# Kernel tuning notes

Hardware: AMD Instinct MI355X
Metric: run time of the kernel (lower is better)

Reference implementation:

```python
import jax, jax.numpy as jnp
import numpy as np

B, T, D = 2, 1024, 768
H, HS = 12, 64          # n_head, head_size = n_embed // n_head
E, K = 8, 1             # num_experts, top-k (MoeLayer default k=1)
DF = 4 * D              # FFN hidden
EPS = 1e-5


def _ln(x, g, b):
    mu = jnp.mean(x, axis=-1, keepdims=True)
    var = jnp.mean(jnp.square(x - mu), axis=-1, keepdims=True)
    return (x - mu) * jax.lax.rsqrt(var + EPS) * g + b


def setup_inputs() -> dict:
    key = jax.random.key(0)
    ks = jax.random.split(key, 12)
    s = 0.02
    return {
        "x": jax.random.normal(ks[0], (B, T, D), dtype=jnp.float32),
        "ln1_g": jnp.ones((D,), jnp.float32),
        "ln1_b": jnp.zeros((D,), jnp.float32),
        "ln2_g": jnp.ones((D,), jnp.float32),
        "ln2_b": jnp.zeros((D,), jnp.float32),
        "Wq": jax.random.normal(ks[1], (H, D, HS), jnp.float32) * s,
        "Wk": jax.random.normal(ks[2], (H, D, HS), jnp.float32) * s,
        "Wv": jax.random.normal(ks[3], (H, D, HS), jnp.float32) * s,
        "Wp": jax.random.normal(ks[4], (D, D), jnp.float32) * s,
        "bp": jnp.zeros((D,), jnp.float32),
        "Wg": jax.random.normal(ks[5], (D, E), jnp.float32) * s,
        "W1": jax.random.normal(ks[6], (E, D, DF), jnp.float32) * s,
        "b1": jnp.zeros((E, DF), jnp.float32),
        "W2": jax.random.normal(ks[7], (E, DF, D), jnp.float32) * s,
        "b2": jnp.zeros((E, D), jnp.float32),
    }


def reference(x, ln1_g, ln1_b, ln2_g, ln2_b, Wq, Wk, Wv, Wp, bp, Wg, W1, b1, W2, b2):
    b, t, d = x.shape

    # ---- multi-head causal self-attention (per-head QKV, as in Head) ----
    h = _ln(x, ln1_g, ln1_b)
    q = jnp.einsum('btd,hds->bhts', h, Wq)
    k = jnp.einsum('btd,hds->bhts', h, Wk)
    v = jnp.einsum('btd,hds->bhts', h, Wv)
    # NOTE: original scales by C**-0.5 with C = n_embed (not head_size)
    scores = jnp.einsum('bhts,bhus->bhtu', q, k) * (d ** -0.5)
    causal = jnp.tril(jnp.ones((t, t), dtype=bool))
    scores = jnp.where(causal, scores, -jnp.inf)
    att = jax.nn.softmax(scores, axis=-1)
    out = jnp.einsum('bhtu,bhus->bhts', att, v)          # [B,H,T,HS]
    out = out.transpose(0, 2, 1, 3).reshape(b, t, d)     # concat heads
    x = x + out @ Wp + bp

    # ---- top-k MoE feed-forward (MoeLayer, k=1) ----
    h2 = _ln(x, ln2_g, ln2_b).reshape(-1, d)             # [N,D]
    gate_logits = h2 @ Wg                                # [N,E]
    w, sel = jax.lax.top_k(gate_logits, K)               # [N,K]
    w = jax.nn.softmax(w.astype(jnp.float32), axis=-1).astype(x.dtype)
    n = h2.shape[0]
    combine = jnp.zeros((n, Wg.shape[1]), x.dtype).at[
        jnp.arange(n)[:, None], sel].add(w)              # [N,E]
    hid = jax.nn.relu(jnp.einsum('nd,edf->enf', h2, W1) + b1[:, None, :])
    y = jnp.einsum('enf,efd->end', hid, W2) + b2[:, None, :]
    moe = jnp.einsum('ne,end->nd', combine, y)           # dense dispatch
    return x + moe.reshape(b, t, d)
```

## Files before the change

### kernel.cpp

```cpp
#include <hip/hip_runtime.h>
#include <math.h>

typedef __bf16 bf16;
typedef __bf16 bf16x4 __attribute__((ext_vector_type(4)));
typedef __bf16 bf16x8 __attribute__((ext_vector_type(8)));
typedef float f32x4 __attribute__((ext_vector_type(4)));

#define N_TOK 2048
#define DMODEL 768
#define NHEAD 12
#define TSEQ 1024
#define NEXP 8
#define DFF 3072

__device__ inline f32x4 mfma16(bf16x8 a, bf16x8 b, f32x4 c) {
    return __builtin_amdgcn_mfma_f32_16x16x32_bf16(a, b, c, 0, 0, 0);
}

__device__ inline f32x4 zero4() { f32x4 z = {0.f, 0.f, 0.f, 0.f}; return z; }

__device__ inline float block_sum(float v, float* red, int tid) {
#pragma unroll
    for (int off = 32; off > 0; off >>= 1) v += __shfl_down(v, off, 64);
    __syncthreads();
    if ((tid & 63) == 0) red[tid >> 6] = v;
    __syncthreads();
    return red[0] + red[1] + red[2] + red[3];
}

__global__ __launch_bounds__(256) void ln1_kernel(const float* __restrict__ x,
        const float* __restrict__ g, const float* __restrict__ b,
        bf16* __restrict__ hh, bf16* __restrict__ hl,
        int* __restrict__ cz, float* __restrict__ outz) {
    __shared__ float red[4];
    int row = blockIdx.x, tid = threadIdx.x;
    if (row == 0 && tid < 16) cz[tid] = 0;
#pragma unroll
    for (int i = 0; i < 3; i++) outz[(size_t)row * DMODEL + tid + i * 256] = 0.f;
    const float* xr = x + (size_t)row * DMODEL;
    float v[3];
#pragma unroll
    for (int i = 0; i < 3; i++) v[i] = xr[tid + i * 256];
    float s = block_sum(v[0] + v[1] + v[2], red, tid);
    float mu = s * (1.f / DMODEL);
    float q = 0.f;
#pragma unroll
    for (int i = 0; i < 3; i++) { float d = v[i] - mu; q += d * d; }
    q = block_sum(q, red, tid);
    float rstd = 1.0f / sqrtf(q * (1.f / DMODEL) + 1e-5f);
#pragma unroll
    for (int i = 0; i < 3; i++) {
        int d = tid + i * 256;
        float val = (v[i] - mu) * rstd * g[d] + b[d];
        bf16 hi = (bf16)val;
        hh[(size_t)row * DMODEL + d] = hi;
        hl[(size_t)row * DMODEL + d] = (bf16)(val - (float)hi);
    }
}

__device__ inline void gemm_step3(const bf16* lah, const bf16* lal,
                                  const bf16* lbh, const bf16* lbl,
                                  int wm, int wn, int row16, int quad,
                                  f32x4 acc[4][4]) {
    bf16x8 ah[4], al[4], bh[4], bl[4];
#pragma unroll
    for (int i = 0; i < 4; i++) {
        int ro = (wm * 64 + i * 16 + row16) * 40 + quad * 8;
        ah[i] = *(const bf16x8*)&lah[ro];
        al[i] = *(const bf16x8*)&lal[ro];
    }
#pragma unroll
    for (int i = 0; i < 4; i++) {
        int ro = (wn * 64 + i * 16 + row16) * 40 + quad * 8;
        bh[i] = *(const bf16x8*)&lbh[ro];
        bl[i] = *(const bf16x8*)&lbl[ro];
    }
#pragma unroll
    for (int mi = 0; mi < 4; mi++)
#pragma unroll
        for (int ni = 0; ni < 4; ni++) {
            acc[mi][ni] = mfma16(ah[mi], bh[ni], acc[mi][ni]);
            acc[mi][ni] = mfma16(ah[mi], bl[ni], acc[mi][ni]);
            acc[mi][ni] = mfma16(al[mi], bh[ni], acc[mi][ni]);
        }
}

__device__ inline void gemm_step1(const bf16* la, const bf16* lb, int wm, int wn,
                                  int row16, int quad, f32x4 acc[4][4]) {
    bf16x8 af[4], bfr[4];
#pragma unroll
    for (int i = 0; i < 4; i++)
        af[i] = *(const bf16x8*)&la[(wm * 64 + i * 16 + row16) * 40 + quad * 8];
#pragma unroll
    for (int i = 0; i < 4; i++)
        bfr[i] = *(const bf16x8*)&lb[(wn * 64 + i * 16 + row16) * 40 + quad * 8];
#pragma unroll
    for (int mi = 0; mi < 4; mi++)
#pragma unroll
        for (int ni = 0; ni < 4; ni++)
            acc[mi][ni] = mfma16(af[mi], bfr[ni], acc[mi][ni]);
}

#define TILE_E (128 * 40)

__device__ inline void wstore_hilo(bf16* lbh, bf16* lbl, int base, const float* wv) {
#pragma unroll
    for (int gq = 0; gq < 4; gq++) {
        bf16x4 ph, pl;
#pragma unroll
        for (int j = 0; j < 4; j++) {
            float v = wv[gq * 4 + j];
            bf16 hi = (bf16)v;
            ph[j] = hi;
            pl[j] = (bf16)(v - (float)hi);
        }
        *(bf16x4*)&lbh[base + gq * 4] = ph;
        *(bf16x4*)&lbl[base + gq * 4] = pl;
    }
}
__device__ inline void wstore1(bf16* lb, int base, const float* wv) {
#pragma unroll
    for (int gq = 0; gq < 4; gq++) {
        bf16x4 p;
#pragma unroll
        for (int j = 0; j < 4; j++) p[j] = (bf16)wv[gq * 4 + j];
        *(bf16x4*)&lb[base + gq * 4] = p;
    }
}

__global__ __launch_bounds__(256) void qkv_gemm(const bf16* __restrict__ hA_h,
        const bf16* __restrict__ hA_l,
        const float* __restrict__ Wq, const float* __restrict__ Wk,
        const float* __restrict__ Wv,
        bf16* __restrict__ qh, bf16* __restrict__ ql,
        bf16* __restrict__ kh, bf16* __restrict__ kl,
        bf16* __restrict__ vh, bf16* __restrict__ vl) {
    __shared__ alignas(16) bf16 lah[2 * TILE_E];
    __shared__ alignas(16) bf16 lal[2 * TILE_E];
    __shared__ alignas(16) bf16 lbh[2 * TILE_E];
    __shared__ alignas(16) bf16 lbl[2 * TILE_E];
    int id = blockIdx.x;
    int nt = id % 24;
    if (nt >= 18) return;
    int m0 = (id / 24) * 128;
    int tid = threadIdx.x;
    int sel = nt / 6;
    int n0 = (nt % 6) * 128;
    const float* W = (sel == 0) ? Wq : (sel == 1) ? Wk : Wv;
    bf16* obh = (sel == 0) ? qh : (sel == 1) ? kh : vh;
    bf16* obl = (sel == 0) ? ql : (sel == 1) ? kl : vl;
    int lane = tid & 63, w = tid >> 6, row16 = lane & 15, quad = lane >> 4;
    int wm = w >> 1, wn = w & 1;
    int r_a = tid >> 2, c_a = (tid & 3) << 3;
    int nW = tid & 127, kb16 = (tid >> 7) * 16;
    size_t wcol = (size_t)((n0 + nW) >> 6) * DMODEL * 64 + ((n0 + nW) & 63);
    int wbase = nW * 40 + kb16;
    f32x4 acc[4][4];
#pragma unroll
    for (int mi = 0; mi < 4; mi++)
#pragma unroll
        for (int ni = 0; ni < 4; ni++) acc[mi][ni] = zero4();
    const bf16* Ah = hA_h + (size_t)m0 * DMODEL;
    const bf16* Al = hA_l + (size_t)m0 * DMODEL;
    bf16x8 rAh0_0, rAh1_0, rAl0_0, rAl1_0, rAh0_1, rAh1_1, rAl0_1, rAl1_1;
    float wv0[16], wv1[16];

#define QK_LOAD(bk, k0) do { \
    rAh0_##bk = *(const bf16x8*)&Ah[(size_t)r_a * DMODEL + (k0) + c_a]; \
    rAh1_##bk = *(const bf16x8*)&Ah[(size_t)(r_a + 64) * DMODEL + (k0) + c_a]; \
    rAl0_##bk = *(const bf16x8*)&Al[(size_t)r_a * DMODEL + (k0) + c_a]; \
    rAl1_##bk = *(const bf16x8*)&Al[(size_t)(r_a + 64) * DMODEL + (k0) + c_a]; \
    _Pragma("unroll") for (int i = 0; i < 16; i++) \
        wv##bk[i] = W[wcol + (size_t)((k0) + kb16 + i) * 64]; \
} while (0)
#define QK_STORE(bk, lofs) do { \
    *(bf16x8*)&lah[(lofs) + r_a * 40 + c_a] = rAh0_##bk; \
    *(bf16x8*)&lah[(lofs) + (r_a + 64) * 40 + c_a] = rAh1_##bk; \
    *(bf16x8*)&lal[(lofs) + r_a * 40 + c_a] = rAl0_##bk; \
    *(bf16x8*)&lal[(lofs) + (r_a + 64) * 40 + c_a] = rAl1_##bk; \
    wstore_hilo(lbh + (lofs), lbl + (lofs), wbase, wv##bk); \
} while (0)

    const int nk = DMODEL / 32;
    QK_LOAD(0, 0);
    QK_LOAD(1, 32);
    QK_STORE(0, 0);
    for (int ki = 0; ki < nk; ki += 2) {
        __syncthreads();
        if (ki + 2 < nk) QK_LOAD(0, (ki + 2) * 32);
        gemm_step3(lah, lal, lbh, lbl, wm, wn, row16, quad, acc);
        QK_STORE(1, TILE_E);
        __syncthreads();
        if (ki + 3 < nk) QK_LOAD(1, (ki + 3) * 32);
        gemm_step3(lah + TILE_E, lal + TILE_E, lbh + TILE_E, lbl + TILE_E,
                   wm, wn, row16, quad, acc);
        if (ki + 2 < nk) QK_STORE(0, 0);
    }
#undef QK_LOAD
#undef QK_STORE
#pragma unroll
    for (int mi = 0; mi < 4; mi++) {
        int rowl = wm * 64 + mi * 16 + quad * 4;
#pragma unroll
        for (int ni = 0; ni < 4; ni++) {
            int col = n0 + wn * 64 + ni * 16 + row16;
            int hhd = col >> 6, s = col & 63;
#pragma unroll
            for (int r = 0; r < 4; r++) {
                int gm = m0 + rowl + r;
                int bb = gm >> 10, t = gm & 1023;
                size_t oi = (((size_t)bb * NHEAD + hhd) * TSEQ + t) * 64 + s;
                float val = acc[mi][ni][r];
                bf16 hi = (bf16)val;
                obh[oi] = hi;
                obl[oi] = (bf16)(val - (float)hi);
            }
        }
    }
}

__global__ __launch_bounds__(256) void attn_kernel(const bf16* __restrict__ qhb,
        const bf16* __restrict__ qlb, const bf16* __restrict__ khb,
        const bf16* __restrict__ klb, const bf16* __restrict__ vhb,
        const bf16* __restrict__ vlb, bf16* __restrict__ aoh,
        bf16* __restrict__ aol) {
    __shared__ alignas(16) bf16 kt_h[64 * 72];
    __shared__ alignas(16) bf16 kt_l[64 * 72];
    __shared__ alignas(16) bf16 vt_h[64 * 72];
    __shared__ alignas(16) bf16 vt_l[64 * 72];
    __shared__ alignas(16) bf16 p_h[4][16 * 72];
    __shared__ alignas(16) bf16 p_l[4][16 * 72];
    int qt = blockIdx.x, bh = blockIdx.y;
    int b = bh / NHEAD, hh = bh % NHEAD;
    int tid = threadIdx.x, lane = tid & 63, w = tid >> 6;
    int row16 = lane & 15, quad = lane >> 4;
    const bf16* qph = qhb + (size_t)bh * TSEQ * 64;
    const bf16* qpl = qlb + (size_t)bh * TSEQ * 64;
    const bf16* kph = khb + (size_t)bh * TSEQ * 64;
    const bf16* kpl = klb + (size_t)bh * TSEQ * 64;
    const bf16* vph = vhb + (size_t)bh * TSEQ * 64;
    const bf16* vpl = vlb + (size_t)bh * TSEQ * 64;
    int qrow = qt * 64 + w * 16 + row16;
    bf16x8 aq_h[2], aq_l[2];
#pragma unroll
    for (int kk = 0; kk < 2; kk++) {
        aq_h[kk] = *(const bf16x8*)&qph[(size_t)qrow * 64 + kk * 32 + quad * 8];
        aq_l[kk] = *(const bf16x8*)&qpl[(size_t)qrow * 64 + kk * 32 + quad * 8];
    }
    f32x4 o[4];
    float m_i[4], l_i[4];
#pragma unroll
    for (int i = 0; i < 4; i++) { o[i] = zero4(); m_i[i] = -INFINITY; l_i[i] = 0.f; }
    const float sc = 0.03608439182435161f;
    for (int kt = 0; kt <= qt; kt++) {
        __syncthreads();
#pragma unroll
        for (int i = 0; i < 2; i++) {
            int chunk = tid + i * 256;
            int r = chunk >> 3, c = (chunk & 7) << 3;
            size_t gi = (size_t)(kt * 64 + r) * 64 + c;
            *(bf16x8*)&kt_h[r * 72 + c] = *(const bf16x8*)&kph[gi];
            *(bf16x8*)&kt_l[r * 72 + c] = *(const bf16x8*)&kpl[gi];
        }
#pragma unroll
        for (int u = 0; u < 4; u++) {
            int unit = tid + u * 256;
            int s = unit & 63, tg = unit >> 6;
            bf16x4 ph, pl;
#pragma unroll
            for (int j = 0; j < 4; j++) {
                size_t gi = (size_t)(kt * 64 + tg * 4 + j) * 64 + s;
                ph[j] = vph[gi];
                pl[j] = vpl[gi];
            }
            *(bf16x4*)&vt_h[s * 72 + tg * 4] = ph;
            *(bf16x4*)&vt_l[s * 72 + tg * 4] = pl;
        }
        __syncthreads();
        f32x4 sacc[4];
#pragma unroll
        for (int ni = 0; ni < 4; ni++) {
            sacc[ni] = zero4();
#pragma unroll
            for (int kk = 0; kk < 2; kk++) {
                int ro = (ni * 16 + row16) * 72 + kk * 32 + quad * 8;
                bf16x8 bk_h = *(const bf16x8*)&kt_h[ro];
                bf16x8 bk_l = *(const bf16x8*)&kt_l[ro];
                sacc[ni] = mfma16(aq_h[kk], bk_h, sacc[ni]);
                sacc[ni] = mfma16(aq_h[kk], bk_l, sacc[ni]);
                sacc[ni] = mfma16(aq_l[kk], bk_h, sacc[ni]);
            }
        }
        float mrow[4];
#pragma unroll
        for (int r = 0; r < 4; r++) mrow[r] = -INFINITY;
        int tq_b = qt * 64 + w * 16 + quad * 4;
#pragma unroll
        for (int ni = 0; ni < 4; ni++) {
            int tkg = kt * 64 + ni * 16 + row16;
#pragma unroll
            for (int r = 0; r < 4; r++) {
                float sv = sacc[ni][r] * sc;
                if (tkg > tq_b + r) sv = -INFINITY;
                sacc[ni][r] = sv;
                mrow[r] = fmaxf(mrow[r], sv);
            }
        }
#pragma unroll
        for (int r = 0; r < 4; r++) {
#pragma unroll
            for (int off = 8; off > 0; off >>= 1)
                mrow[r] = fmaxf(mrow[r], __shfl_xor(mrow[r], off, 16));
        }
        float alpha[4], rsum[4];
#pragma unroll
        for (int r = 0; r < 4; r++) {
            float nm = fmaxf(m_i[r], mrow[r]);
            alpha[r] = __expf(m_i[r] - nm);
            m_i[r] = nm;
            rsum[r] = 0.f;
        }
#pragma unroll
        for (int ni = 0; ni < 4; ni++)
#pragma unroll
            for (int r = 0; r < 4; r++) {
                float p = __expf(sacc[ni][r] - m_i[r]);
                sacc[ni][r] = p;
                rsum[r] += p;
            }
#pragma unroll
        for (int r = 0; r < 4; r++) {
#pragma unroll
            for (int off = 8; off > 0; off >>= 1)
                rsum[r] += __shfl_xor(rsum[r], off, 16);
            l_i[r] = l_i[r] * alpha[r] + rsum[r];
        }
#pragma unroll
        for (int ni = 0; ni < 4; ni++)
#pragma unroll
            for (int r = 0; r < 4; r++) o[ni][r] *= alpha[r];
#pragma unroll
        for (int ni = 0; ni < 4; ni++)
#pragma unroll
            for (int r = 0; r < 4; r++) {
                float p = sacc[ni][r];
                bf16 hi = (bf16)p;
                int po = (quad * 4 + r) * 72 + ni * 16 + row16;
                p_h[w][po] = hi;
                p_l[w][po] = (bf16)(p - (float)hi);
            }
        __syncthreads();
        bf16x8 ap_h[2], ap_l[2];
#pragma unroll
        for (int kk = 0; kk < 2; kk++) {
            ap_h[kk] = *(const bf16x8*)&p_h[w][row16 * 72 + kk * 32 + quad * 8];
            ap_l[kk] = *(const bf16x8*)&p_l[w][row16 * 72 + kk * 32 + quad * 8];
        }
#pragma unroll
        for (int ni = 0; ni < 4; ni++)
#pragma unroll
            for (int kk = 0; kk < 2; kk++) {
                int ro = (ni * 16 + row16) * 72 + kk * 32 + quad * 8;
                bf16x8 bv_h = *(const bf16x8*)&vt_h[ro];
                bf16x8 bv_l = *(const bf16x8*)&vt_l[ro];
                o[ni] = mfma16(ap_h[kk], bv_h, o[ni]);
                o[ni] = mfma16(ap_h[kk], bv_l, o[ni]);
                o[ni] = mfma16(ap_l[kk], bv_h, o[ni]);
            }
    }
    int t = qt * 64 + w * 16 + quad * 4;
#pragma unroll
    for (int ni = 0; ni < 4; ni++) {
        int col = hh * 64 + ni * 16 + row16;
#pragma unroll
        for (int r = 0; r < 4; r++) {
            float val = o[ni][r] / l_i[r];
            size_t n = (size_t)b * TSEQ + t + r;
            bf16 hi = (bf16)val;
            aoh[n * DMODEL + col] = hi;
            aol[n * DMODEL + col] = (bf16)(val - (float)hi);
        }
    }
}

__global__ __launch_bounds__(256) void proj_gemm(const bf16* __restrict__ aInH,
        const bf16* __restrict__ aInL,
        const float* __restrict__ Wp, const float* __restrict__ bp,
        const float* __restrict__ x, float* __restrict__ x1) {
    __shared__ alignas(16) bf16 lah[2 * TILE_E];
    __shared__ alignas(16) bf16 lal[2 * TILE_E];
    __shared__ alignas(16) bf16 lbh[2 * TILE_E];
    __shared__ alignas(16) bf16 lbl[2 * TILE_E];
    int id = blockIdx.x;
    int n0t = id & 7;
    if (n0t >= 6) return;
    int m0 = (id >> 3) * 128, n0 = n0t * 128;
    int tid = threadIdx.x;
    int lane = tid & 63, w = tid >> 6, row16 = lane & 15, quad = lane >> 4;
    int wm = w >> 1, wn = w & 1;
    int r_a = tid >> 2, c_a = (tid & 3) << 3;
    int nW = tid & 127, kb16 = (tid >> 7) * 16;
    int wbase = nW * 40 + kb16;
    f32x4 acc[4][4];
#pragma unroll
    for (int mi = 0; mi < 4; mi++)
#pragma unroll
        for (int ni = 0; ni < 4; ni++) acc[mi][ni] = zero4();
    const bf16* Ah = aInH + (size_t)m0 * DMODEL;
    const bf16* Al = aInL + (size_t)m0 * DMODEL;
    bf16x8 rAh0_0, rAh1_0, rAl0_0, rAl1_0, rAh0_1, rAh1_1, rAl0_1, rAl1_1;
    float wv0[16], wv1[16];

#define PJ_LOAD(bk, k0) do { \
    rAh0_##bk = *(const bf16x8*)&Ah[(size_t)r_a * DMODEL + (k0) + c_a]; \
    rAh1_##bk = *(const bf16x8*)&Ah[(size_t)(r_a + 64) * DMODEL + (k0) + c_a]; \
    rAl0_##bk = *(const bf16x8*)&Al[(size_t)r_a * DMODEL + (k0) + c_a]; \
    rAl1_##bk = *(const bf16x8*)&Al[(size_t)(r_a + 64) * DMODEL + (k0) + c_a]; \
    _Pragma("unroll") for (int i = 0; i < 16; i++) \
        wv##bk[i] = Wp[(size_t)((k0) + kb16 + i) * DMODEL + n0 + nW]; \
} while (0)
#define PJ_STORE(bk, lofs) do { \
    *(bf16x8*)&lah[(lofs) + r_a * 40 + c_a] = rAh0_##bk; \
    *(bf16x8*)&lah[(lofs) + (r_a + 64) * 40 + c_a] = rAh1_##bk; \
    *(bf16x8*)&lal[(lofs) + r_a * 40 + c_a] = rAl0_##bk; \
    *(bf16x8*)&lal[(lofs) + (r_a + 64) * 40 + c_a] = rAl1_##bk; \
    wstore_hilo(lbh + (lofs), lbl + (lofs), wbase, wv##bk); \
} while (0)

    const int nk = DMODEL / 32;
    PJ_LOAD(0, 0);
    PJ_LOAD(1, 32);
    PJ_STORE(0, 0);
    for (int ki = 0; ki < nk; ki += 2) {
        __syncthreads();
        if (ki + 2 < nk) PJ_LOAD(0, (ki + 2) * 32);
        gemm_step3(lah, lal, lbh, lbl, wm, wn, row16, quad, acc);
        PJ_STORE(1, TILE_E);
        __syncthreads();
        if (ki + 3 < nk) PJ_LOAD(1, (ki + 3) * 32);
        gemm_step3(lah + TILE_E, lal + TILE_E, lbh + TILE_E, lbl + TILE_E,
                   wm, wn, row16, quad, acc);
        if (ki + 2 < nk) PJ_STORE(0, 0);
    }
#undef PJ_LOAD
#undef PJ_STORE
#pragma unroll
    for (int mi = 0; mi < 4; mi++) {
        int rowl = wm * 64 + mi * 16 + quad * 4;
#pragma unroll
        for (int ni = 0; ni < 4; ni++) {
            int col = n0 + wn * 64 + ni * 16 + row16;
#pragma unroll
            for (int r = 0; r < 4; r++) {
                int gm = m0 + rowl + r;
                x1[(size_t)gm * DMODEL + col] =
                    acc[mi][ni][r] + bp[col] + x[(size_t)gm * DMODEL + col];
            }
        }
    }
}

__global__ __launch_bounds__(256) void ln2_gate_kernel(const float* __restrict__ x1,
        const float* __restrict__ g, const float* __restrict__ b,
        const float* __restrict__ Wg, bf16* __restrict__ h2,
        int* __restrict__ sel, int* __restrict__ counts) {
    __shared__ float red[4];
    __shared__ float glog[8];
    int row = blockIdx.x, tid = threadIdx.x;
    if (tid < 8) glog[tid] = 0.f;
    const float* xr = x1 + (size_t)row * DMODEL;
    float v[3];
#pragma unroll
    for (int i = 0; i < 3; i++) v[i] = xr[tid + i * 256];
    float s = block_sum(v[0] + v[1] + v[2], red, tid);
    float mu = s * (1.f / DMODEL);
    float qv = 0.f;
#pragma unroll
    for (int i = 0; i < 3; i++) { float d = v[i] - mu; qv += d * d; }
    qv = block_sum(qv, red, tid);
    float rstd = 1.0f / sqrtf(qv * (1.f / DMODEL) + 1e-5f);
    float ga[8];
#pragma unroll
    for (int e = 0; e < 8; e++) ga[e] = 0.f;
#pragma unroll
    for (int i = 0; i < 3; i++) {
        int d = tid + i * 256;
        float hv = (v[i] - mu) * rstd * g[d] + b[d];
        h2[(size_t)row * DMODEL + d] = (bf16)hv;
        const float* wgr = Wg + (size_t)d * NEXP;
#pragma unroll
        for (int e = 0; e < 8; e++) ga[e] += hv * wgr[e];
    }
#pragma unroll
    for (int e = 0; e < 8; e++)
#pragma unroll
        for (int off = 32; off > 0; off >>= 1) ga[e] += __shfl_down(ga[e], off, 64);
    if ((tid & 63) == 0)
#pragma unroll
        for (int e = 0; e < 8; e++) atomicAdd(&glog[e], ga[e]);
    __syncthreads();
    if (tid == 0) {
        float best = glog[0];
        int bi = 0;
#pragma unroll
        for (int e = 1; e < 8; e++)
            if (glog[e] > best) { best = glog[e]; bi = e; }
        sel[row] = bi;
        atomicAdd(&counts[bi], 1);
    }
}

__global__ void scatter_kernel(const int* __restrict__ sel, const int* __restrict__ counts,
                               int* __restrict__ cursor, int* __restrict__ perm) {
    int n = blockIdx.x * blockDim.x + threadIdx.x;
    if (n >= N_TOK) return;
    int e = sel[n];
    int off = 0;
    for (int i = 0; i < NEXP; i++) off += (i < e) ? counts[i] : 0;
    int pos = atomicAdd(&cursor[e], 1);
    perm[off + pos] = n;
}

__global__ __launch_bounds__(256) void moe1_gemm(const bf16* __restrict__ h2,
        const float* __restrict__ W1, const float* __restrict__ b1,
        const int* __restrict__ counts, const int* __restrict__ perm,
        bf16* __restrict__ hid) {
    int e = blockIdx.z;
    int cnt = counts[e];
    int rt = blockIdx.y;
    if (rt * 128 >= cnt) return;
    int off = 0;
    for (int i = 0; i < NEXP; i++) off += (i < e) ? counts[i] : 0;
    int n0 = blockIdx.x * 128;
    const float* W = W1 + (size_t)e * DMODEL * DFF;
    __shared__ alignas(16) bf16 la[2 * TILE_E];
    __shared__ alignas(16) bf16 lb[2 * TILE_E];
    int tid = threadIdx.x;
    int lane = tid & 63, w = tid >> 6, row16 = lane & 15, quad = lane >> 4;
    int wm = w >> 1, wn = w & 1;
    int r_a = tid >> 2, c_a = (tid & 3) << 3;
    int nW = tid & 127, kb16 = (tid >> 7) * 16;
    int wbase = nW * 40 + kb16;
    int tok0 = perm[off + min(rt * 128 + r_a, cnt - 1)];
    int tok1 = perm[off + min(rt * 128 + r_a + 64, cnt - 1)];
    const bf16* a0 = h2 + (size_t)tok0 * DMODEL;
    const bf16* a1 = h2 + (size_t)tok1 * DMODEL;
    f32x4 acc[4][4];
#pragma unroll
    for (int mi = 0; mi < 4; mi++)
#pragma unroll
        for (int ni = 0; ni < 4; ni++) acc[mi][ni] = zero4();
    bf16x8 rA0_0, rA1_0, rA0_1, rA1_1;
    float wv0[16], wv1[16];

#define M1_LOAD(bk, k0) do { \
    rA0_##bk = *(const bf16x8*)&a0[(k0) + c_a]; \
    rA1_##bk = *(const bf16x8*)&a1[(k0) + c_a]; \
    _Pragma("unroll") for (int i = 0; i < 16; i++) \
        wv##bk[i] = W[(size_t)((k0) + kb16 + i) * DFF + n0 + nW]; \
} while (0)
#define M1_STORE(bk, lofs) do { \
    *(bf16x8*)&la[(lofs) + r_a * 40 + c_a] = rA0_##bk; \
    *(bf16x8*)&la[(lofs) + (r_a + 64) * 40 + c_a] = rA1_##bk; \
    wstore1(lb + (lofs), wbase, wv##bk); \
} while (0)

    const int nk = DMODEL / 32;
    M1_LOAD(0, 0);
    M1_LOAD(1, 32);
    M1_STORE(0, 0);
    for (int ki = 0; ki < nk; ki += 2) {
        __syncthreads();
        if (ki + 2 < nk) M1_LOAD(0, (ki + 2) * 32);
        gemm_step1(la, lb, wm, wn, row16, quad, acc);
        M1_STORE(1, TILE_E);
        __syncthreads();
        if (ki + 3 < nk) M1_LOAD(1, (ki + 3) * 32);
        gemm_step1(la + TILE_E, lb + TILE_E, wm, wn, row16, quad, acc);
        if (ki + 2 < nk) M1_STORE(0, 0);
    }
#undef M1_LOAD
#undef M1_STORE
#pragma unroll
    for (int mi = 0; mi < 4; mi++) {
        int rowl = wm * 64 + mi * 16 + quad * 4;
#pragma unroll
        for (int ni = 0; ni < 4; ni++) {
            int col = n0 + wn * 64 + ni * 16 + row16;
#pragma unroll
            for (int r = 0; r < 4; r++) {
                int lr = rowl + r;
                if (rt * 128 + lr < cnt) {
                    float val = acc[mi][ni][r] + b1[(size_t)e * DFF + col];
                    val = fmaxf(val, 0.f);
                    hid[(size_t)(off + rt * 128 + lr) * DFF + col] = (bf16)val;
                }
            }
        }
    }
}

__global__ __launch_bounds__(256) void moe2_gemm(const bf16* __restrict__ hid,
        const float* __restrict__ W2, const float* __restrict__ b2,
        const int* __restrict__ counts, const int* __restrict__ perm,
        const float* __restrict__ x1, float* __restrict__ out) {
    int id = blockIdx.x;
    int n0t = id & 7;
    if (n0t >= 6) return;
    int rt = (id >> 3) & 15;
    int ez = id >> 7;
    int e = ez & 7, ks = ez >> 3;
    int cnt = counts[e];
    if (rt * 128 >= cnt) return;
    int off = 0;
    for (int i = 0; i < NEXP; i++) off += (i < e) ? counts[i] : 0;
    int n0 = n0t * 128;
    const float* W = W2 + (size_t)e * DFF * DMODEL;
    __shared__ alignas(16) bf16 la[2 * TILE_E];
    __shared__ alignas(16) bf16 lb[2 * TILE_E];
    int tid = threadIdx.x;
    int lane = tid & 63, w = tid >> 6, row16 = lane & 15, quad = lane >> 4;
    int wm = w >> 1, wn = w & 1;
    int r_a = tid >> 2, c_a = (tid & 3) << 3;
    int nW = tid & 127, kb16 = (tid >> 7) * 16;
    int wbase = nW * 40 + kb16;
    const int kst = ks * (DFF / 4);
    const bf16* a0 = hid + (size_t)min(off + rt * 128 + r_a, N_TOK - 1) * DFF + kst;
    const bf16* a1 = hid + (size_t)min(off + rt * 128 + r_a + 64, N_TOK - 1) * DFF + kst;
    const float* Wk_ = W + (size_t)kst * DMODEL;
    f32x4 acc[4][4];
#pragma unroll
    for (int mi = 0; mi < 4; mi++)
#pragma unroll
        for (int ni = 0; ni < 4; ni++) acc[mi][ni] = zero4();
    bf16x8 rA0_0, rA1_0, rA0_1, rA1_1;
    float wv0[16], wv1[16];

#define M2_LOAD(bk, k0) do { \
    rA0_##bk = *(const bf16x8*)&a0[(k0) + c_a]; \
    rA1_##bk = *(const bf16x8*)&a1[(k0) + c_a]; \
    _Pragma("unroll") for (int i = 0; i < 16; i++) \
        wv##bk[i] = Wk_[(size_t)((k0) + kb16 + i) * DMODEL + n0 + nW]; \
} while (0)
#define M2_STORE(bk, lofs) do { \
    *(bf16x8*)&la[(lofs) + r_a * 40 + c_a] = rA0_##bk; \
    *(bf16x8*)&la[(lofs) + (r_a + 64) * 40 + c_a] = rA1_##bk; \
    wstore1(lb + (lofs), wbase, wv##bk); \
} while (0)

    const int nk = (DFF / 4) / 32;
    M2_LOAD(0, 0);
    M2_LOAD(1, 32);
    M2_STORE(0, 0);
    for (int ki = 0; ki < nk; ki += 2) {
        __syncthreads();
        if (ki + 2 < nk) M2_LOAD(0, (ki + 2) * 32);
        gemm_step1(la, lb, wm, wn, row16, quad, acc);
        M2_STORE(1, TILE_E);
        __syncthreads();
        if (ki + 3 < nk) M2_LOAD(1, (ki + 3) * 32);
        gemm_step1(la + TILE_E, lb + TILE_E, wm, wn, row16, quad, acc);
        if (ki + 2 < nk) M2_STORE(0, 0);
    }
#undef M2_LOAD
#undef M2_STORE
#pragma unroll
    for (int mi = 0; mi < 4; mi++) {
        int rowl = wm * 64 + mi * 16 + quad * 4;
#pragma unroll
        for (int ni = 0; ni < 4; ni++) {
            int col = n0 + wn * 64 + ni * 16 + row16;
#pragma unroll
            for (int r = 0; r < 4; r++) {
                int lr = rowl + r;
                if (rt * 128 + lr < cnt) {
                    int n = perm[off + rt * 128 + lr];
                    float val = acc[mi][ni][r];
                    if (ks == 0)
                        val += b2[(size_t)e * DMODEL + col] + x1[(size_t)n * DMODEL + col];
                    atomicAdd(&out[(size_t)n * DMODEL + col], val);
                }
            }
        }
    }
}

extern "C" void kernel_launch(void* const* d_in, const int* in_sizes, int n_in,
                              void* d_out, int out_size, void* d_ws, size_t ws_size,
                              hipStream_t stream) {
    const float* x    = (const float*)d_in[0];
    const float* ln1g = (const float*)d_in[1];
    const float* ln1b = (const float*)d_in[2];
    const float* ln2g = (const float*)d_in[3];
    const float* ln2b = (const float*)d_in[4];
    const float* Wq   = (const float*)d_in[5];
    const float* Wk   = (const float*)d_in[6];
    const float* Wv   = (const float*)d_in[7];
    const float* Wp   = (const float*)d_in[8];
    const float* bp   = (const float*)d_in[9];
    const float* Wg   = (const float*)d_in[10];
    const float* W1   = (const float*)d_in[11];
    const float* b1   = (const float*)d_in[12];
    const float* W2   = (const float*)d_in[13];
    const float* b2   = (const float*)d_in[14];
    float* out = (float*)d_out;

    char* ws = (char*)d_ws;
    size_t off = 0;
    const size_t SZ = (size_t)N_TOK * DMODEL * 2;
    bf16* h1h = (bf16*)(ws + off); off += SZ;
    bf16* h1l = (bf16*)(ws + off); off += SZ;
    bf16* qh  = (bf16*)(ws + off); off += SZ;
    bf16* ql  = (bf16*)(ws + off); off += SZ;
    bf16* kh  = (bf16*)(ws + off); off += SZ;
    bf16* kl  = (bf16*)(ws + off); off += SZ;
    bf16* vh  = (bf16*)(ws + off); off += SZ;
    bf16* vl  = (bf16*)(ws + off); off += SZ;
    bf16* aoh = (bf16*)(ws + off); off += SZ;
    bf16* aol = (bf16*)(ws + off); off += SZ;
    float* x1 = (float*)(ws + off); off += (size_t)N_TOK * DMODEL * 4;
    bf16* h2  = (bf16*)(ws + off); off += SZ;
    bf16* hid = (bf16*)(ws + off); off += (size_t)N_TOK * DFF * 2;
    int* counts  = (int*)(ws + off); off += 8 * 4;
    int* cursor  = (int*)(ws + off); off += 8 * 4;
    int* sel     = (int*)(ws + off); off += (size_t)N_TOK * 4;
    int* perm    = (int*)(ws + off); off += (size_t)N_TOK * 4;

    ln1_kernel<<<N_TOK, 256, 0, stream>>>(x, ln1g, ln1b, h1h, h1l, counts, out);
    qkv_gemm<<<24 * 16, 256, 0, stream>>>(h1h, h1l, Wq, Wk, Wv, qh, ql, kh, kl, vh, vl);
    attn_kernel<<<dim3(16, 24), 256, 0, stream>>>(qh, ql, kh, kl, vh, vl, aoh, aol);
    proj_gemm<<<8 * 16, 256, 0, stream>>>(aoh, aol, Wp, bp, x, x1);
    ln2_gate_kernel<<<N_TOK, 256, 0, stream>>>(x1, ln2g, ln2b, Wg, h2, sel, counts);
    scatter_kernel<<<8, 256, 0, stream>>>(sel, counts, cursor, perm);
    moe1_gemm<<<dim3(24, 16, 8), 256, 0, stream>>>(h2, W1, b1, counts, perm, hid);
    moe2_gemm<<<8 * 16 * 32, 256, 0, stream>>>(hid, W2, b2, counts, perm, x1, out);
}
```

Baseline: 625.5 us.

## Pre-pack MoE expert weights into bf16 tiled layout and simplify GEMM pipelines

Adds a pack_w kernel that runs every call and converts the fp32 W1/W2 expert weights into bf16, transposed and tiled into contiguous 32x128 blocks. The MoE GEMMs then load B tiles with two vectorized 16-byte loads per thread instead of sixteen strided fp32 loads, and they no longer convert to bf16 inside the loop. All GEMM main loops are also restructured from a two-register-set, two-step unrolled pipeline to a single register set with ping-pong shared-memory buffers, which lowers register pressure. The cost is that packing reads and writes all expert weights each call, roughly 150MB fp32 read, even though only the routed experts' rows are used.

```diff
diff --git a/kernel.cpp b/kernel.cpp
--- a/kernel.cpp
+++ b/kernel.cpp
@@ -58,6 +58,37 @@
     }
 }
 
+__global__ __launch_bounds__(256) void pack_w(const float* __restrict__ src,
+        bf16* __restrict__ dst, int K, int N) {
+    int kt = blockIdx.x, nt = blockIdx.y, e = blockIdx.z;
+    int nkt = gridDim.x;
+    const float* S = src + ((size_t)e * K + kt * 32) * N + nt * 128;
+    bf16* D = dst + (((size_t)e * gridDim.y + nt) * nkt + kt) * 4096;
+    __shared__ float t[32][129];
+    int tid = threadIdx.x;
+    int kk = tid >> 4, nn = (tid & 15) * 8;
+#pragma unroll
+    for (int h = 0; h < 2; h++) {
+        int k = kk + 16 * h;
+        float4 v0 = *(const float4*)&S[(size_t)k * N + nn];
+        float4 v1 = *(const float4*)&S[(size_t)k * N + nn + 4];
+        t[k][nn + 0] = v0.x; t[k][nn + 1] = v0.y;
+        t[k][nn + 2] = v0.z; t[k][nn + 3] = v0.w;
+        t[k][nn + 4] = v1.x; t[k][nn + 5] = v1.y;
+        t[k][nn + 6] = v1.z; t[k][nn + 7] = v1.w;
+    }
+    __syncthreads();
+    int n = tid >> 1, kh = (tid & 1) * 16;
+    bf16x8 o0, o1;
+#pragma unroll
+    for (int j = 0; j < 8; j++) {
+        o0[j] = (bf16)t[kh + j][n];
+        o1[j] = (bf16)t[kh + 8 + j][n];
+    }
+    *(bf16x8*)&D[n * 32 + kh] = o0;
+    *(bf16x8*)&D[n * 32 + kh + 8] = o1;
+}
+
 __device__ inline void gemm_step3(const bf16* lah, const bf16* lal,
                                   const bf16* lbh, const bf16* lbl,
                                   int wm, int wn, int row16, int quad,
@@ -116,15 +147,6 @@
         }
         *(bf16x4*)&lbh[base + gq * 4] = ph;
         *(bf16x4*)&lbl[base + gq * 4] = pl;
-    }
-}
-__device__ inline void wstore1(bf16* lb, int base, const float* wv) {
-#pragma unroll
-    for (int gq = 0; gq < 4; gq++) {
-        bf16x4 p;
-#pragma unroll
-        for (int j = 0; j < 4; j++) p[j] = (bf16)wv[gq * 4 + j];
-        *(bf16x4*)&lb[base + gq * 4] = p;
     }
 }
 
@@ -162,39 +184,34 @@
         for (int ni = 0; ni < 4; ni++) acc[mi][ni] = zero4();
     const bf16* Ah = hA_h + (size_t)m0 * DMODEL;
     const bf16* Al = hA_l + (size_t)m0 * DMODEL;
-    bf16x8 rAh0_0, rAh1_0, rAl0_0, rAl1_0, rAh0_1, rAh1_1, rAl0_1, rAl1_1;
-    float wv0[16], wv1[16];
-
-#define QK_LOAD(bk, k0) do { \
-    rAh0_##bk = *(const bf16x8*)&Ah[(size_t)r_a * DMODEL + (k0) + c_a]; \
-    rAh1_##bk = *(const bf16x8*)&Ah[(size_t)(r_a + 64) * DMODEL + (k0) + c_a]; \
-    rAl0_##bk = *(const bf16x8*)&Al[(size_t)r_a * DMODEL + (k0) + c_a]; \
-    rAl1_##bk = *(const bf16x8*)&Al[(size_t)(r_a + 64) * DMODEL + (k0) + c_a]; \
+    bf16x8 rAh0, rAh1, rAl0, rAl1;
+    float wv[16];
+
+#define QK_LOAD(k0) do { \
+    rAh0 = *(const bf16x8*)&Ah[(size_t)r_a * DMODEL + (k0) + c_a]; \
+    rAh1 = *(const bf16x8*)&Ah[(size_t)(r_a + 64) * DMODEL + (k0) + c_a]; \
+    rAl0 = *(const bf16x8*)&Al[(size_t)r_a * DMODEL + (k0) + c_a]; \
+    rAl1 = *(const bf16x8*)&Al[(size_t)(r_a + 64) * DMODEL + (k0) + c_a]; \
     _Pragma("unroll") for (int i = 0; i < 16; i++) \
-        wv##bk[i] = W[wcol + (size_t)((k0) + kb16 + i) * 64]; \
+        wv[i] = W[wcol + (size_t)((k0) + kb16 + i) * 64]; \
 } while (0)
-#define QK_STORE(bk, lofs) do { \
-    *(bf16x8*)&lah[(lofs) + r_a * 40 + c_a] = rAh0_##bk; \
-    *(bf16x8*)&lah[(lofs) + (r_a + 64) * 40 + c_a] = rAh1_##bk; \
-    *(bf16x8*)&lal[(lofs) + r_a * 40 + c_a] = rAl0_##bk; \
-    *(bf16x8*)&lal[(lofs) + (r_a + 64) * 40 + c_a] = rAl1_##bk; \
-    wstore_hilo(lbh + (lofs), lbl + (lofs), wbase, wv##bk); \
+#define QK_STORE(lofs) do { \
+    *(bf16x8*)&lah[(lofs) + r_a * 40 + c_a] = rAh0; \
+    *(bf16x8*)&lah[(lofs) + (r_a + 64) * 40 + c_a] = rAh1; \
+    *(bf16x8*)&lal[(lofs) + r_a * 40 + c_a] = rAl0; \
+    *(bf16x8*)&lal[(lofs) + (r_a + 64) * 40 + c_a] = rAl1; \
+    wstore_hilo(lbh + (lofs), lbl + (lofs), wbase, wv); \
 } while (0)
 
     const int nk = DMODEL / 32;
-    QK_LOAD(0, 0);
-    QK_LOAD(1, 32);
-    QK_STORE(0, 0);
-    for (int ki = 0; ki < nk; ki += 2) {
+    QK_LOAD(0);
+    QK_STORE(0);
+    for (int ki = 0; ki < nk; ki++) {
         __syncthreads();
-        if (ki + 2 < nk) QK_LOAD(0, (ki + 2) * 32);
-        gemm_step3(lah, lal, lbh, lbl, wm, wn, row16, quad, acc);
-        QK_STORE(1, TILE_E);
-        __syncthreads();
-        if (ki + 3 < nk) QK_LOAD(1, (ki + 3) * 32);
-        gemm_step3(lah + TILE_E, lal + TILE_E, lbh + TILE_E, lbl + TILE_E,
-                   wm, wn, row16, quad, acc);
-        if (ki + 2 < nk) QK_STORE(0, 0);
+        int cur = (ki & 1) * TILE_E, nxt = ((ki + 1) & 1) * TILE_E;
+        if (ki + 1 < nk) QK_LOAD((ki + 1) * 32);
+        gemm_step3(lah + cur, lal + cur, lbh + cur, lbl + cur, wm, wn, row16, quad, acc);
+        if (ki + 1 < nk) QK_STORE(nxt);
     }
 #undef QK_LOAD
 #undef QK_STORE
@@ -408,39 +425,34 @@
         for (int ni = 0; ni < 4; ni++) acc[mi][ni] = zero4();
     const bf16* Ah = aInH + (size_t)m0 * DMODEL;
     const bf16* Al = aInL + (size_t)m0 * DMODEL;
-    bf16x8 rAh0_0, rAh1_0, rAl0_0, rAl1_0, rAh0_1, rAh1_1, rAl0_1, rAl1_1;
-    float wv0[16], wv1[16];
-
-#define PJ_LOAD(bk, k0) do { \
-    rAh0_##bk = *(const bf16x8*)&Ah[(size_t)r_a * DMODEL + (k0) + c_a]; \
-    rAh1_##bk = *(const bf16x8*)&Ah[(size_t)(r_a + 64) * DMODEL + (k0) + c_a]; \
-    rAl0_##bk = *(const bf16x8*)&Al[(size_t)r_a * DMODEL + (k0) + c_a]; \
-    rAl1_##bk = *(const bf16x8*)&Al[(size_t)(r_a + 64) * DMODEL + (k0) + c_a]; \
+    bf16x8 rAh0, rAh1, rAl0, rAl1;
+    float wv[16];
+
+#define PJ_LOAD(k0) do { \
+    rAh0 = *(const bf16x8*)&Ah[(size_t)r_a * DMODEL + (k0) + c_a]; \
+    rAh1 = *(const bf16x8*)&Ah[(size_t)(r_a + 64) * DMODEL + (k0) + c_a]; \
+    rAl0 = *(const bf16x8*)&Al[(size_t)r_a * DMODEL + (k0) + c_a]; \
+    rAl1 = *(const bf16x8*)&Al[(size_t)(r_a + 64) * DMODEL + (k0) + c_a]; \
     _Pragma("unroll") for (int i = 0; i < 16; i++) \
-        wv##bk[i] = Wp[(size_t)((k0) + kb16 + i) * DMODEL + n0 + nW]; \
+        wv[i] = Wp[(size_t)((k0) + kb16 + i) * DMODEL + n0 + nW]; \
 } while (0)
-#define PJ_STORE(bk, lofs) do { \
-    *(bf16x8*)&lah[(lofs) + r_a * 40 + c_a] = rAh0_##bk; \
-    *(bf16x8*)&lah[(lofs) + (r_a + 64) * 40 + c_a] = rAh1_##bk; \
-    *(bf16x8*)&lal[(lofs) + r_a * 40 + c_a] = rAl0_##bk; \
-    *(bf16x8*)&lal[(lofs) + (r_a + 64) * 40 + c_a] = rAl1_##bk; \
-    wstore_hilo(lbh + (lofs), lbl + (lofs), wbase, wv##bk); \
+#define PJ_STORE(lofs) do { \
+    *(bf16x8*)&lah[(lofs) + r_a * 40 + c_a] = rAh0; \
+    *(bf16x8*)&lah[(lofs) + (r_a + 64) * 40 + c_a] = rAh1; \
+    *(bf16x8*)&lal[(lofs) + r_a * 40 + c_a] = rAl0; \
+    *(bf16x8*)&lal[(lofs) + (r_a + 64) * 40 + c_a] = rAl1; \
+    wstore_hilo(lbh + (lofs), lbl + (lofs), wbase, wv); \
 } while (0)
 
     const int nk = DMODEL / 32;
-    PJ_LOAD(0, 0);
-    PJ_LOAD(1, 32);
-    PJ_STORE(0, 0);
-    for (int ki = 0; ki < nk; ki += 2) {
+    PJ_LOAD(0);
+    PJ_STORE(0);
+    for (int ki = 0; ki < nk; ki++) {
         __syncthreads();
-        if (ki + 2 < nk) PJ_LOAD(0, (ki + 2) * 32);
-        gemm_step3(lah, lal, lbh, lbl, wm, wn, row16, quad, acc);
-        PJ_STORE(1, TILE_E);
-        __syncthreads();
-        if (ki + 3 < nk) PJ_LOAD(1, (ki + 3) * 32);
-        gemm_step3(lah + TILE_E, lal + TILE_E, lbh + TILE_E, lbl + TILE_E,
-                   wm, wn, row16, quad, acc);
-        if (ki + 2 < nk) PJ_STORE(0, 0);
+        int cur = (ki & 1) * TILE_E, nxt = ((ki + 1) & 1) * TILE_E;
+        if (ki + 1 < nk) PJ_LOAD((ki + 1) * 32);
+        gemm_step3(lah + cur, lal + cur, lbh + cur, lbl + cur, wm, wn, row16, quad, acc);
+        if (ki + 1 < nk) PJ_STORE(nxt);
     }
 #undef PJ_LOAD
 #undef PJ_STORE
@@ -522,7 +534,7 @@
 }
 
 __global__ __launch_bounds__(256) void moe1_gemm(const bf16* __restrict__ h2,
-        const float* __restrict__ W1, const float* __restrict__ b1,
+        const bf16* __restrict__ W1t, const float* __restrict__ b1,
         const int* __restrict__ counts, const int* __restrict__ perm,
         bf16* __restrict__ hid) {
     int e = blockIdx.z;
@@ -531,16 +543,16 @@
     if (rt * 128 >= cnt) return;
     int off = 0;
     for (int i = 0; i < NEXP; i++) off += (i < e) ? counts[i] : 0;
-    int n0 = blockIdx.x * 128;
-    const float* W = W1 + (size_t)e * DMODEL * DFF;
+    int nt = blockIdx.x;
+    int n0 = nt * 128;
+    const bf16* T = W1t + ((size_t)(e * 24 + nt) * 24) * 4096;
     __shared__ alignas(16) bf16 la[2 * TILE_E];
     __shared__ alignas(16) bf16 lb[2 * TILE_E];
     int tid = threadIdx.x;
     int lane = tid & 63, w = tid >> 6, row16 = lane & 15, quad = lane >> 4;
     int wm = w >> 1, wn = w & 1;
     int r_a = tid >> 2, c_a = (tid & 3) << 3;
-    int nW = tid & 127, kb16 = (tid >> 7) * 16;
-    int wbase = nW * 40 + kb16;
+    int bn = tid >> 1, bk = (tid & 1) * 16;
     int tok0 = perm[off + min(rt * 128 + r_a, cnt - 1)];
     int tok1 = perm[off + min(rt * 128 + r_a + 64, cnt - 1)];
     const bf16* a0 = h2 + (size_t)tok0 * DMODEL;
@@ -550,34 +562,30 @@
     for (int mi = 0; mi < 4; mi++)
 #pragma unroll
         for (int ni = 0; ni < 4; ni++) acc[mi][ni] = zero4();
-    bf16x8 rA0_0, rA1_0, rA0_1, rA1_1;
-    float wv0[16], wv1[16];
-
-#define M1_LOAD(bk, k0) do { \
-    rA0_##bk = *(const bf16x8*)&a0[(k0) + c_a]; \
-    rA1_##bk = *(const bf16x8*)&a1[(k0) + c_a]; \
-    _Pragma("unroll") for (int i = 0; i < 16; i++) \
-        wv##bk[i] = W[(size_t)((k0) + kb16 + i) * DFF + n0 + nW]; \
+    bf16x8 rA0, rA1, rB0, rB1;
+
+#define M1_LOAD(kt) do { \
+    rA0 = *(const bf16x8*)&a0[(kt) * 32 + c_a]; \
+    rA1 = *(const bf16x8*)&a1[(kt) * 32 + c_a]; \
+    rB0 = *(const bf16x8*)&T[(size_t)(kt) * 4096 + tid * 16]; \
+    rB1 = *(const bf16x8*)&T[(size_t)(kt) * 4096 + tid * 16 + 8]; \
 } while (0)
-#define M1_STORE(bk, lofs) do { \
-    *(bf16x8*)&la[(lofs) + r_a * 40 + c_a] = rA0_##bk; \
-    *(bf16x8*)&la[(lofs) + (r_a + 64) * 40 + c_a] = rA1_##bk; \
-    wstore1(lb + (lofs), wbase, wv##bk); \
+#define M1_STORE(lofs) do { \
+    *(bf16x8*)&la[(lofs) + r_a * 40 + c_a] = rA0; \
+    *(bf16x8*)&la[(lofs) + (r_a + 64) * 40 + c_a] = rA1; \
+    *(bf16x8*)&lb[(lofs) + bn * 40 + bk] = rB0; \
+    *(bf16x8*)&lb[(lofs) + bn * 40 + bk + 8] = rB1; \
 } while (0)
 
     const int nk = DMODEL / 32;
-    M1_LOAD(0, 0);
-    M1_LOAD(1, 32);
-    M1_STORE(0, 0);
-    for (int ki = 0; ki < nk; ki += 2) {
+    M1_LOAD(0);
+    M1_STORE(0);
+    for (int ki = 0; ki < nk; ki++) {
         __syncthreads();
-        if (ki + 2 < nk) M1_LOAD(0, (ki + 2) * 32);
-        gemm_step1(la, lb, wm, wn, row16, quad, acc);
-        M1_STORE(1, TILE_E);
-        __syncthreads();
-        if (ki + 3 < nk) M1_LOAD(1, (ki + 3) * 32);
-        gemm_step1(la + TILE_E, lb + TILE_E, wm, wn, row16, quad, acc);
-        if (ki + 2 < nk) M1_STORE(0, 0);
+        int cur = (ki & 1) * TILE_E, nxt = ((ki + 1) & 1) * TILE_E;
+        if (ki + 1 < nk) M1_LOAD(ki + 1);
+        gemm_step1(la + cur, lb + cur, wm, wn, row16, quad, acc);
+        if (ki + 1 < nk) M1_STORE(nxt);
     }
 #undef M1_LOAD
 #undef M1_STORE
@@ -601,7 +609,7 @@
 }
 
 __global__ __launch_bounds__(256) void moe2_gemm(const bf16* __restrict__ hid,
-        const float* __restrict__ W2, const float* __restrict__ b2,
+        const bf16* __restrict__ W2t, const float* __restrict__ b2,
         const int* __restrict__ counts, const int* __restrict__ perm,
         const float* __restrict__ x1, float* __restrict__ out) {
     int id = blockIdx.x;
@@ -615,52 +623,46 @@
     int off = 0;
     for (int i = 0; i < NEXP; i++) off += (i < e) ? counts[i] : 0;
     int n0 = n0t * 128;
-    const float* W = W2 + (size_t)e * DFF * DMODEL;
+    const bf16* T = W2t + ((size_t)(e * 6 + n0t) * 96 + ks * 24) * 4096;
     __shared__ alignas(16) bf16 la[2 * TILE_E];
     __shared__ alignas(16) bf16 lb[2 * TILE_E];
     int tid = threadIdx.x;
     int lane = tid & 63, w = tid >> 6, row16 = lane & 15, quad = lane >> 4;
     int wm = w >> 1, wn = w & 1;
     int r_a = tid >> 2, c_a = (tid & 3) << 3;
-    int nW = tid & 127, kb16 = (tid >> 7) * 16;
-    int wbase = nW * 40 + kb16;
+    int bn = tid >> 1, bk = (tid & 1) * 16;
     const int kst = ks * (DFF / 4);
     const bf16* a0 = hid + (size_t)min(off + rt * 128 + r_a, N_TOK - 1) * DFF + kst;
     const bf16* a1 = hid + (size_t)min(off + rt * 128 + r_a + 64, N_TOK - 1) * DFF + kst;
-    const float* Wk_ = W + (size_t)kst * DMODEL;
     f32x4 acc[4][4];
 #pragma unroll
     for (int mi = 0; mi < 4; mi++)
 #pragma unroll
         for (int ni = 0; ni < 4; ni++) acc[mi][ni] = zero4();
-    bf16x8 rA0_0, rA1_0, rA0_1, rA1_1;
-    float wv0[16], wv1[16];
-
-#define M2_LOAD(bk, k0) do { \
-    rA0_##bk = *(const bf16x8*)&a0[(k0) + c_a]; \
-    rA1_##bk = *(const bf16x8*)&a1[(k0) + c_a]; \
-    _Pragma("unroll") for (int i = 0; i < 16; i++) \
-        wv##bk[i] = Wk_[(size_t)((k0) + kb16 + i) * DMODEL + n0 + nW]; \
+    bf16x8 rA0, rA1, rB0, rB1;
+
+#define M2_LOAD(kt) do { \
+    rA0 = *(const bf16x8*)&a0[(kt) * 32 + c_a]; \
+    rA1 = *(const bf16x8*)&a1[(kt) * 32 + c_a]; \
+    rB0 = *(const bf16x8*)&T[(size_t)(kt) * 4096 + tid * 16]; \
+    rB1 = *(const bf16x8*)&T[(size_t)(kt) * 4096 + tid * 16 + 8]; \
 } while (0)
-#define M2_STORE(bk, lofs) do { \
-    *(bf16x8*)&la[(lofs) + r_a * 40 + c_a] = rA0_##bk; \
-    *(bf16x8*)&la[(lofs) + (r_a + 64) * 40 + c_a] = rA1_##bk; \
-    wstore1(lb + (lofs), wbase, wv##bk); \
+#define M2_STORE(lofs) do { \
+    *(bf16x8*)&la[(lofs) + r_a * 40 + c_a] = rA0; \
+    *(bf16x8*)&la[(lofs) + (r_a + 64) * 40 + c_a] = rA1; \
+    *(bf16x8*)&lb[(lofs) + bn * 40 + bk] = rB0; \
+    *(bf16x8*)&lb[(lofs) + bn * 40 + bk + 8] = rB1; \
 } while (0)
 
     const int nk = (DFF / 4) / 32;
-    M2_LOAD(0, 0);
-    M2_LOAD(1, 32);
-    M2_STORE(0, 0);
-    for (int ki = 0; ki < nk; ki += 2) {
+    M2_LOAD(0);
+    M2_STORE(0);
+    for (int ki = 0; ki < nk; ki++) {
         __syncthreads();
-        if (ki + 2 < nk) M2_LOAD(0, (ki + 2) * 32);
-        gemm_step1(la, lb, wm, wn, row16, quad, acc);
-        M2_STORE(1, TILE_E);
-        __syncthreads();
-        if (ki + 3 < nk) M2_LOAD(1, (ki + 3) * 32);
-        gemm_step1(la + TILE_E, lb + TILE_E, wm, wn, row16, quad, acc);
-        if (ki + 2 < nk) M2_STORE(0, 0);
+        int cur = (ki & 1) * TILE_E, nxt = ((ki + 1) & 1) * TILE_E;
+        if (ki + 1 < nk) M2_LOAD(ki + 1);
+        gemm_step1(la + cur, lb + cur, wm, wn, row16, quad, acc);
+        if (ki + 1 < nk) M2_STORE(nxt);
     }
 #undef M2_LOAD
 #undef M2_STORE
@@ -721,17 +723,21 @@
     float* x1 = (float*)(ws + off); off += (size_t)N_TOK * DMODEL * 4;
     bf16* h2  = (bf16*)(ws + off); off += SZ;
     bf16* hid = (bf16*)(ws + off); off += (size_t)N_TOK * DFF * 2;
+    bf16* w1t = (bf16*)(ws + off); off += (size_t)NEXP * DMODEL * DFF * 2;
+    bf16* w2t = (bf16*)(ws + off); off += (size_t)NEXP * DFF * DMODEL * 2;
     int* counts  = (int*)(ws + off); off += 8 * 4;
     int* cursor  = (int*)(ws + off); off += 8 * 4;
     int* sel     = (int*)(ws + off); off += (size_t)N_TOK * 4;
     int* perm    = (int*)(ws + off); off += (size_t)N_TOK * 4;
 
     ln1_kernel<<<N_TOK, 256, 0, stream>>>(x, ln1g, ln1b, h1h, h1l, counts, out);
+    pack_w<<<dim3(DMODEL / 32, DFF / 128, NEXP), 256, 0, stream>>>(W1, w1t, DMODEL, DFF);
+    pack_w<<<dim3(DFF / 32, DMODEL / 128, NEXP), 256, 0, stream>>>(W2, w2t, DFF, DMODEL);
     qkv_gemm<<<24 * 16, 256, 0, stream>>>(h1h, h1l, Wq, Wk, Wv, qh, ql, kh, kl, vh, vl);
     attn_kernel<<<dim3(16, 24), 256, 0, stream>>>(qh, ql, kh, kl, vh, vl, aoh, aol);
     proj_gemm<<<8 * 16, 256, 0, stream>>>(aoh, aol, Wp, bp, x, x1);
     ln2_gate_kernel<<<N_TOK, 256, 0, stream>>>(x1, ln2g, ln2b, Wg, h2, sel, counts);
     scatter_kernel<<<8, 256, 0, stream>>>(sel, counts, cursor, perm);
-    moe1_gemm<<<dim3(24, 16, 8), 256, 0, stream>>>(h2, W1, b1, counts, perm, hid);
-    moe2_gemm<<<8 * 16 * 32, 256, 0, stream>>>(hid, W2, b2, counts, perm, x1, out);
-}
+    moe1_gemm<<<dim3(24, 16, 8), 256, 0, stream>>>(h2, w1t, b1, counts, perm, hid);
+    moe2_gemm<<<8 * 16 * 32, 256, 0, stream>>>(hid, w2t, b2, counts, perm, x1, out);
+}
```

New measurement: 535.3 us. 14.4% less time.
